# Performance work log

Measured on AMD Instinct MI355X. Metric: run time of the kernel, lower is better.

The kernel has to match this reference:

```python
import jax, jax.numpy as jnp
import numpy as np

ALPHA = 0.2            # LeakyReLU negative slope
N, NFEAT, NHID, NHEADS, NCLASS = 270, 4096, 1024, 8, 8
N_DRUG, N_MIC = 175, 95


def setup_inputs() -> dict:
    key = jax.random.key(0)
    ks = jax.random.split(key, 9)
    return {
        "x": jax.random.normal(ks[0], (N, NFEAT), jnp.float32),
        "adj": jax.random.randint(ks[1], (N, N), 0, 2, jnp.int32),
        # per-head GAT parameters, stacked on a leading head axis
        "W": jax.random.normal(ks[2], (NHEADS, NFEAT, NHID), jnp.float32) * 0.02,
        "a_src": jax.random.normal(ks[3], (NHEADS, NHID), jnp.float32) * 0.02,
        "a_dst": jax.random.normal(ks[4], (NHEADS, NHID), jnp.float32) * 0.02,
        # output attention layer (concat=False)
        "W_out": jax.random.normal(ks[5], (NHEADS * NHID, NCLASS), jnp.float32) * 0.02,
        "a_out_src": jax.random.normal(ks[6], (NCLASS,), jnp.float32) * 0.02,
        "a_out_dst": jax.random.normal(ks[7], (NCLASS,), jnp.float32) * 0.02,
        # bilinear score matrix alpha1 (nclass, nclass)
        "alpha1": jax.random.normal(ks[8], (NCLASS, NCLASS), jnp.float32) * 0.3,
    }


def _gat_layer(h_in, mask, W, a_src, a_dst):
    """pyGAT sparse attention layer, expressed densely with an adjacency mask.

    edge weight e_ij = exp(-leakyrelu(a_src.h_i + a_dst.h_j)) for adj[i,j]!=0,
    h'_i = sum_j e_ij h_j / sum_j e_ij   (dropout=0 -> identity on edge weights)
    """
    h = h_in @ W                                             # (N, D)
    logits = (h @ a_src)[:, None] + (h @ a_dst)[None, :]     # (N, N)
    e = jnp.exp(-jax.nn.leaky_relu(logits, ALPHA)) * mask    # masked edge weights
    return (e @ h) / e.sum(axis=1, keepdims=True)            # (N, D)


def reference(x, adj, W, a_src, a_dst, W_out, a_out_src, a_out_dst, alpha1):
    mask = adj.astype(x.dtype)
    # multi-head attention, concat=True -> elu applied inside each head
    heads = jax.vmap(_gat_layer, in_axes=(None, None, 0, 0, 0))(
        x, mask, W, a_src, a_dst)                            # (H, N, nhid)
    h = jax.nn.elu(heads)
    h = jnp.transpose(h, (1, 0, 2)).reshape(N, NHEADS * NHID)  # torch.cat(dim=1)
    # output attention layer (concat=False), elu applied by SpGAT.forward
    out = jax.nn.elu(_gat_layer(h, mask, W_out, a_out_src, a_out_dst))  # (N, nclass)
    # the 270-iteration python copy loop == a static split at row 175
    drug_k = out[:N_DRUG]                                    # (175, 8)
    mic_k = out[N_DRUG:N_DRUG + N_MIC]                       # (95, 8)
    return (drug_k @ alpha1) @ mic_k.T                       # (175, 95)
```

## Files before the change

kernel.cpp:

```cpp
#include <hip/hip_runtime.h>
#include <hip/hip_bf16.h>

#define NN     270
#define MPAD   320
#define NFEAT  4096
#define NHID   1024
#define NHEADS 8
#define NCLS   8
#define NDRUG  175
#define NMIC   95
#define LALPHA 0.2f

typedef unsigned short u16;
typedef unsigned int   u32;
typedef __attribute__((ext_vector_type(8))) short bf16x8;
typedef __attribute__((ext_vector_type(4))) short bf16x4;
typedef __attribute__((ext_vector_type(4))) float f32x4;

static __device__ __forceinline__ u16 f2bf(float f) {
  union { float f; u32 u; } v; v.f = f;
  u32 r = v.u + 0x7FFFu + ((v.u >> 16) & 1u);
  return (u16)(r >> 16);
}
static __device__ __forceinline__ float bf2f(u16 b) {
  union { u32 u; float f; } v; v.u = ((u32)b) << 16;
  return v.f;
}
static __device__ __forceinline__ float wave_red(float v) {
  #pragma unroll
  for (int o = 32; o > 0; o >>= 1) v += __shfl_down(v, o, 64);
  return v;
}
static __device__ __forceinline__ void block_sync() {
  asm volatile("" ::: "memory");
  __builtin_amdgcn_s_barrier();
  asm volatile("" ::: "memory");
}
#define GLOAD16(g, l) __builtin_amdgcn_global_load_lds(                    \
    (__attribute__((address_space(1))) void*)(g),                          \
    (__attribute__((address_space(3))) void*)(l), 16, 0, 0)

__global__ void cvt_x(const float* __restrict__ x, u16* __restrict__ xb) {
  int i = (blockIdx.x * 256 + threadIdx.x) * 8;
  if (i >= MPAD * NFEAT) return;
  int row = i >> 12;
  uint4 o = {0, 0, 0, 0};
  if (row < NN) {
    float4 a = *(const float4*)(x + i);
    float4 b = *(const float4*)(x + i + 4);
    o.x = (u32)f2bf(a.x) | ((u32)f2bf(a.y) << 16);
    o.y = (u32)f2bf(a.z) | ((u32)f2bf(a.w) << 16);
    o.z = (u32)f2bf(b.x) | ((u32)f2bf(b.y) << 16);
    o.w = (u32)f2bf(b.z) | ((u32)f2bf(b.w) << 16);
  }
  *(uint4*)(xb + i) = o;
}

__global__ __launch_bounds__(256, 2) void gemm1(const u16* __restrict__ xb,
                                                const float* __restrict__ W,
                                                u16* __restrict__ Hpart) {
  __shared__ __align__(16) u16   lA[2][MPAD * 32];
  __shared__ __align__(16) float lWf[3][32 * 64];
  __shared__ __align__(16) u32   lWbf[2][1024];
  const int tid  = threadIdx.x;
  const int lane = tid & 63;
  const int wv   = tid >> 6;
  const int b    = blockIdx.x;
  const int ntile = b >> 2;
  const int ks    = b & 3;
  const int head  = ntile >> 4;
  const int jB    = (ntile & 15) * 64;

  const char* gA0 = (const char*)xb + (tid >> 2) * 8192 + ks * 2048
                    + (((tid & 3) ^ ((tid >> 3) & 3)) << 4);
  const char* gW0 = (const char*)W + (size_t)head * 16777216 + (size_t)ks * 4194304
                    + (tid >> 4) * 4096 + jB * 4 + ((tid & 15) << 4);

  auto issueA = [&](int j) {
    char* l0 = (char*)&lA[j & 1][0] + tid * 16;
    const char* g0 = gA0 + j * 64;
    #pragma unroll
    for (int s = 0; s < 5; ++s)
      GLOAD16(g0 + s * 524288, l0 + s * 4096);
  };
  auto issueW = [&](int j) {
    char* l0 = (char*)&lWf[j % 3][0] + tid * 16;
    const char* g0 = gW0 + j * 131072;
    GLOAD16(g0, l0);
    GLOAD16(g0 + 65536, l0 + 4096);
  };
  const int tcol = tid & 63;
  const int tkb  = tid >> 6;
  auto transposeW = [&](int j) {
    const float* wf = &lWf[j % 3][0];
    float f[8];
    #pragma unroll
    for (int q = 0; q < 8; ++q) f[q] = wf[(tkb * 8 + q) * 64 + tcol];
    uint4 o;
    o.x = (u32)f2bf(f[0]) | ((u32)f2bf(f[1]) << 16);
    o.y = (u32)f2bf(f[2]) | ((u32)f2bf(f[3]) << 16);
    o.z = (u32)f2bf(f[4]) | ((u32)f2bf(f[5]) << 16);
    o.w = (u32)f2bf(f[6]) | ((u32)f2bf(f[7]) << 16);
    *(uint4*)((char*)&lWbf[j & 1][0] + tkb * 1024 + tcol * 16) = o;
  };

  f32x4 acc[5][4];
  #pragma unroll
  for (int m = 0; m < 5; ++m)
    #pragma unroll
    for (int n = 0; n < 4; ++n) acc[m][n] = (f32x4){0.f, 0.f, 0.f, 0.f};

  issueW(0); issueW(1); issueA(0); issueA(1); issueW(2);
  asm volatile("s_waitcnt vmcnt(14)" ::: "memory");
  block_sync();
  transposeW(0);
  asm volatile("s_waitcnt lgkmcnt(0)" ::: "memory");

  const int lc = lane & 15;
  const int lg = lane >> 4;
  for (int j = 0; j < 32; ++j) {
    if (j <= 29)      asm volatile("s_waitcnt vmcnt(7)" ::: "memory");
    else if (j == 30) asm volatile("s_waitcnt vmcnt(5)" ::: "memory");
    else              asm volatile("s_waitcnt vmcnt(0)" ::: "memory");
    block_sync();

    {
      const char* aB = (const char*)&lA[j & 1][0];
      const char* bB = (const char*)&lWbf[j & 1][0];
      bf16x8 bfr[4];
      #pragma unroll
      for (int n = 0; n < 4; ++n)
        bfr[n] = *(const bf16x8*)(bB + lg * 1024 + (n * 16 + lc) * 16);
      #pragma unroll
      for (int m = 0; m < 5; ++m) {
        const int row = wv * 80 + m * 16 + lc;
        bf16x8 afr = *(const bf16x8*)(aB + row * 64 + ((lg ^ ((row >> 1) & 3)) << 4));
        #pragma unroll
        for (int n = 0; n < 4; ++n)
          acc[m][n] = __builtin_amdgcn_mfma_f32_16x16x32_bf16(afr, bfr[n], acc[m][n], 0, 0, 0);
      }
      if (j < 31) transposeW(j + 1);
    }
    asm volatile("s_waitcnt lgkmcnt(0)" ::: "memory");
    block_sync();
    if (j <= 29) issueA(j + 2);
    if (j <= 28) issueW(j + 3);
  }

  u16* hp = Hpart + (size_t)ks * (NN * 8192) + (size_t)(ntile * 64);
  #pragma unroll
  for (int m = 0; m < 5; ++m)
    #pragma unroll
    for (int r = 0; r < 4; ++r) {
      const int row = wv * 80 + m * 16 + (lg << 2) + r;
      if (row < NN) {
        #pragma unroll
        for (int n = 0; n < 4; ++n)
          hp[(size_t)row * 8192 + n * 16 + lc] = f2bf(acc[m][n][r]);
      }
    }
}

__global__ void srcdstf(const u16* __restrict__ Hp, const float* __restrict__ a_src,
                        const float* __restrict__ a_dst, u16* __restrict__ Hb,
                        float* __restrict__ srcv, float* __restrict__ dstv) {
  const int i = blockIdx.x, h = blockIdx.y;
  const int tid = threadIdx.x;
  const int j4 = tid * 4;
  const u16* base = Hp + (size_t)i * 8192 + h * 1024 + j4;
  float4 v = {0.f, 0.f, 0.f, 0.f};
  #pragma unroll
  for (int q = 0; q < 4; ++q) {
    bf16x4 p = *(const bf16x4*)(base + (size_t)q * (NN * 8192));
    v.x += bf2f((u16)p[0]); v.y += bf2f((u16)p[1]);
    v.z += bf2f((u16)p[2]); v.w += bf2f((u16)p[3]);
  }
  u16* hb = Hb + ((size_t)h * NN + i) * NHID + j4;
  ushort4 hv = { f2bf(v.x), f2bf(v.y), f2bf(v.z), f2bf(v.w) };
  *(ushort4*)hb = hv;
  const float4 as4 = *(const float4*)(a_src + h * NHID + j4);
  const float4 ad4 = *(const float4*)(a_dst + h * NHID + j4);
  float s = v.x * as4.x + v.y * as4.y + v.z * as4.z + v.w * as4.w;
  float d = v.x * ad4.x + v.y * ad4.y + v.z * ad4.z + v.w * ad4.w;
  s = wave_red(s); d = wave_red(d);
  __shared__ float rb[8];
  const int lane = tid & 63, wid = tid >> 6;
  if (lane == 0) { rb[wid] = s; rb[4 + wid] = d; }
  __syncthreads();
  if (tid == 0) {
    srcv[h * NN + i] = rb[0] + rb[1] + rb[2] + rb[3];
    dstv[h * NN + i] = rb[4] + rb[5] + rb[6] + rb[7];
  }
}

__global__ void ekern(const int* __restrict__ adj, const float* __restrict__ srcv,
                      const float* __restrict__ dstv, u16* __restrict__ eb,
                      float* __restrict__ rowsum) {
  const int i = blockIdx.x, h = blockIdx.y;
  const int n = threadIdx.x;
  float ev = 0.f;
  if (n < NN && adj[i * NN + n] != 0) {
    float lg = srcv[h * NN + i] + dstv[h * NN + n];
    float lr = lg > 0.f ? lg : LALPHA * lg;
    ev = expf(-lr);
  }
  u16 evb = f2bf(ev);
  eb[(size_t)h * NN * 320 + (size_t)i * 320 + n] = evb;
  float evr = wave_red(bf2f(evb));
  __shared__ float rb[5];
  const int lane = threadIdx.x & 63, wid = threadIdx.x >> 6;
  if (lane == 0) rb[wid] = evr;
  __syncthreads();
  if (threadIdx.x == 0) rowsum[h * NN + i] = rb[0] + rb[1] + rb[2] + rb[3] + rb[4];
}

__global__ __launch_bounds__(512) void gemm2(const u16* __restrict__ eb,
                                             const u16* __restrict__ Hb,
                                             const float* __restrict__ rowsum,
                                             float* __restrict__ h2) {
  __shared__ __align__(16) u16 lA[320 * 72];
  __shared__ __align__(16) u16 lB[32 * 72];
  const int tid  = threadIdx.x;
  const int lane = tid & 63;
  const int wid  = tid >> 6;
  const int wm   = wid >> 1;
  const int wn   = wid & 1;
  const int head = blockIdx.x >> 5;
  const int j0   = (blockIdx.x & 31) * 32;
  f32x4 acc[5];
  #pragma unroll
  for (int m = 0; m < 5; ++m) acc[m] = (f32x4){0.f, 0.f, 0.f, 0.f};

  for (int k0 = 0; k0 < 320; k0 += 64) {
    __syncthreads();
    #pragma unroll
    for (int it = 0; it < 5; ++it) {
      int f   = tid + it * 512;
      int row = f >> 3;
      int kc  = (f & 7) << 3;
      bf16x8 v = {0,0,0,0,0,0,0,0};
      if (row < NN) v = *(const bf16x8*)(eb + (size_t)head * NN * 320 + (size_t)row * 320 + k0 + kc);
      *(bf16x8*)(lA + row * 72 + kc) = v;
    }
    {
      int kk2 = tid >> 3;
      int jc2 = (tid & 7) << 2;
      int k   = k0 + kk2;
      u16 v0 = 0, v1 = 0, v2 = 0, v3 = 0;
      if (k < NN) {
        bf16x4 hv = *(const bf16x4*)(Hb + (size_t)head * NN * NHID + (size_t)k * NHID + j0 + jc2);
        v0 = (u16)hv[0]; v1 = (u16)hv[1]; v2 = (u16)hv[2]; v3 = (u16)hv[3];
      }
      lB[(jc2 + 0) * 72 + kk2] = v0;
      lB[(jc2 + 1) * 72 + kk2] = v1;
      lB[(jc2 + 2) * 72 + kk2] = v2;
      lB[(jc2 + 3) * 72 + kk2] = v3;
    }
    __syncthreads();
    #pragma unroll
    for (int sub = 0; sub < 2; ++sub) {
      int ksub = sub * 32 + ((lane >> 4) << 3);
      bf16x8 bfrag = *(const bf16x8*)(lB + (wn * 16 + (lane & 15)) * 72 + ksub);
      #pragma unroll
      for (int m = 0; m < 5; ++m) {
        int row = wm * 80 + m * 16 + (lane & 15);
        bf16x8 afrag = *(const bf16x8*)(lA + row * 72 + ksub);
        acc[m] = __builtin_amdgcn_mfma_f32_16x16x32_bf16(afrag, bfrag, acc[m], 0, 0, 0);
      }
    }
  }
  const int jj = j0 + wn * 16 + (lane & 15);
  #pragma unroll
  for (int m = 0; m < 5; ++m) {
    #pragma unroll
    for (int r = 0; r < 4; ++r) {
      int row = wm * 80 + m * 16 + ((lane >> 4) << 2) + r;
      if (row < NN) {
        float v = acc[m][r] / rowsum[head * NN + row];
        v = v > 0.f ? v : expm1f(v);
        h2[(size_t)row * (NHEADS * NHID) + head * NHID + jj] = v;
      }
    }
  }
}

__global__ void layer2(const float* __restrict__ h2, const float* __restrict__ Wout,
                       const float* __restrict__ aos, const float* __restrict__ aod,
                       float* __restrict__ hL2, float* __restrict__ src2,
                       float* __restrict__ dst2) {
  const int i = blockIdx.x;
  float acc[8] = {0,0,0,0,0,0,0,0};
  for (int k = threadIdx.x; k < NHEADS * NHID; k += 256) {
    float hv = h2[(size_t)i * (NHEADS * NHID) + k];
    const float4 w0 = *(const float4*)(Wout + (size_t)k * 8);
    const float4 w1 = *(const float4*)(Wout + (size_t)k * 8 + 4);
    acc[0] += hv * w0.x; acc[1] += hv * w0.y; acc[2] += hv * w0.z; acc[3] += hv * w0.w;
    acc[4] += hv * w1.x; acc[5] += hv * w1.y; acc[6] += hv * w1.z; acc[7] += hv * w1.w;
  }
  #pragma unroll
  for (int c = 0; c < 8; ++c) acc[c] = wave_red(acc[c]);
  __shared__ float rb[4][8];
  const int lane = threadIdx.x & 63, wid = threadIdx.x >> 6;
  if (lane == 0) {
    #pragma unroll
    for (int c = 0; c < 8; ++c) rb[wid][c] = acc[c];
  }
  __syncthreads();
  if (threadIdx.x == 0) {
    float s = 0.f, d = 0.f;
    #pragma unroll
    for (int c = 0; c < 8; ++c) {
      float v = rb[0][c] + rb[1][c] + rb[2][c] + rb[3][c];
      hL2[i * 8 + c] = v;
      s += v * aos[c];
      d += v * aod[c];
    }
    src2[i] = s; dst2[i] = d;
  }
}

__global__ void out2k(const int* __restrict__ adj, const float* __restrict__ src2,
                      const float* __restrict__ dst2, const float* __restrict__ hL2,
                      float* __restrict__ out2) {
  const int i = blockIdx.x;
  float se = 0.f, acc[8] = {0,0,0,0,0,0,0,0};
  for (int n = threadIdx.x; n < NN; n += 256) {
    if (adj[i * NN + n] != 0) {
      float lg = src2[i] + dst2[n];
      float lr = lg > 0.f ? lg : LALPHA * lg;
      float ev = expf(-lr);
      se += ev;
      #pragma unroll
      for (int c = 0; c < 8; ++c) acc[c] += ev * hL2[n * 8 + c];
    }
  }
  se = wave_red(se);
  #pragma unroll
  for (int c = 0; c < 8; ++c) acc[c] = wave_red(acc[c]);
  __shared__ float rb[4][9];
  const int lane = threadIdx.x & 63, wid = threadIdx.x >> 6;
  if (lane == 0) {
    #pragma unroll
    for (int c = 0; c < 8; ++c) rb[wid][c] = acc[c];
    rb[wid][8] = se;
  }
  __syncthreads();
  if (threadIdx.x == 0) {
    float s = rb[0][8] + rb[1][8] + rb[2][8] + rb[3][8];
    #pragma unroll
    for (int c = 0; c < 8; ++c) {
      float v = (rb[0][c] + rb[1][c] + rb[2][c] + rb[3][c]) / s;
      out2[i * 8 + c] = v > 0.f ? v : expm1f(v);
    }
  }
}

__global__ void finalk(const float* __restrict__ out2, const float* __restrict__ alpha1,
                       float* __restrict__ out) {
  int t = blockIdx.x * 256 + threadIdx.x;
  if (t >= NDRUG * NMIC) return;
  int d = t / NMIC, m = t % NMIC;
  const float* dr = out2 + d * 8;
  const float* mi = out2 + (NDRUG + m) * 8;
  float r = 0.f;
  #pragma unroll
  for (int c2 = 0; c2 < 8; ++c2) {
    float a = 0.f;
    #pragma unroll
    for (int c1 = 0; c1 < 8; ++c1) a += dr[c1] * alpha1[c1 * 8 + c2];
    r += a * mi[c2];
  }
  out[t] = r;
}

extern "C" void kernel_launch(void* const* d_in, const int* in_sizes, int n_in,
                              void* d_out, int out_size, void* d_ws, size_t ws_size,
                              hipStream_t stream) {
  const float* x      = (const float*)d_in[0];
  const int*   adj    = (const int*)d_in[1];
  const float* W      = (const float*)d_in[2];
  const float* a_src  = (const float*)d_in[3];
  const float* a_dst  = (const float*)d_in[4];
  const float* W_out  = (const float*)d_in[5];
  const float* aos    = (const float*)d_in[6];
  const float* aod    = (const float*)d_in[7];
  const float* alpha1 = (const float*)d_in[8];
  float* out = (float*)d_out;

  char* p = (char*)d_ws;
  auto take = [&](size_t bytes) {
    char* q = p;
    p += (bytes + 255) & ~(size_t)255;
    return q;
  };
  u16*   xb    = (u16*)  take((size_t)MPAD * NFEAT * 2);
  u16*   Hpart = (u16*)  take((size_t)4 * NN * 8192 * 2);
  u16*   Hb    = (u16*)  take((size_t)NHEADS * NN * NHID * 2);
  float* srcv  = (float*)take((size_t)NHEADS * NN * 4);
  float* dstv  = (float*)take((size_t)NHEADS * NN * 4);
  char*  hbase = (char*)Hpart;
  float* h2    = (float*)hbase;
  u16*   eb    = (u16*)  (hbase + 10000000);
  float* rs    = (float*)(hbase + 11500000);
  float* hL2   = (float*)(hbase + 11600000);
  float* s2    = (float*)(hbase + 11700000);
  float* d2    = (float*)(hbase + 11800000);
  float* o2    = (float*)(hbase + 11900000);

  cvt_x<<<640, 256, 0, stream>>>(x, xb);
  gemm1<<<512, 256, 0, stream>>>(xb, W, Hpart);
  srcdstf<<<dim3(NN, NHEADS), 256, 0, stream>>>(Hpart, a_src, a_dst, Hb, srcv, dstv);
  ekern<<<dim3(NN, NHEADS), 320, 0, stream>>>(adj, srcv, dstv, eb, rs);
  gemm2<<<256, 512, 0, stream>>>(eb, Hb, rs, h2);
  layer2<<<NN, 256, 0, stream>>>(h2, W_out, aos, aod, hL2, s2, d2);
  out2k<<<NN, 256, 0, stream>>>(adj, s2, d2, hL2, o2);
  finalk<<<65, 256, 0, stream>>>(o2, alpha1, out);
}
```

Baseline: 91.77 us.

## Split gemm1 M dimension into three 128-row tiles with XCD-aware block mapping

gemm1 now splits the padded 384-row M dimension into three 128-row tiles, with each wave owning a 64x32 sub-tile. This triples the grid to 1536 blocks, lowers per-block LDS and registers, and raises occupancy from 2 to 3 blocks per CU. Blocks are remapped so that all blocks sharing an N tile sit on the same XCD, aiming for better L2 reuse of W. The cost is that W is now fetched three times, once per M tile, and more of the M work is padding (384 rows vs 320).

```diff
diff --git a/kernel.cpp b/kernel.cpp
--- a/kernel.cpp
+++ b/kernel.cpp
@@ -2,7 +2,7 @@
 #include <hip/hip_bf16.h>
 
 #define NN     270
-#define MPAD   320
+#define MPAD   384
 #define NFEAT  4096
 #define NHID   1024
 #define NHEADS 8
@@ -56,32 +56,37 @@
   *(uint4*)(xb + i) = o;
 }
 
-__global__ __launch_bounds__(256, 2) void gemm1(const u16* __restrict__ xb,
+__global__ __launch_bounds__(256, 3) void gemm1(const u16* __restrict__ xb,
                                                 const float* __restrict__ W,
                                                 u16* __restrict__ Hpart) {
-  __shared__ __align__(16) u16   lA[2][MPAD * 32];
+  __shared__ __align__(16) u16   lA[2][128 * 32];
   __shared__ __align__(16) float lWf[3][32 * 64];
   __shared__ __align__(16) u32   lWbf[2][1024];
   const int tid  = threadIdx.x;
   const int lane = tid & 63;
   const int wv   = tid >> 6;
-  const int b    = blockIdx.x;
-  const int ntile = b >> 2;
-  const int ks    = b & 3;
+  const int wm   = wv >> 1;
+  const int wn   = wv & 1;
+  const int bid   = blockIdx.x;
+  const int xcd   = bid & 7;
+  const int local = bid >> 3;
+  const int ntile = xcd * 16 + local / 12;
+  const int r12   = local % 12;
+  const int mt    = r12 % 3;
+  const int ks    = r12 / 3;
   const int head  = ntile >> 4;
   const int jB    = (ntile & 15) * 64;
 
-  const char* gA0 = (const char*)xb + (tid >> 2) * 8192 + ks * 2048
-                    + (((tid & 3) ^ ((tid >> 3) & 3)) << 4);
+  const char* gA0 = (const char*)xb + (size_t)(mt * 128 + (tid >> 2)) * 8192
+                    + ks * 2048 + (((tid & 3) ^ ((tid >> 3) & 3)) << 4);
   const char* gW0 = (const char*)W + (size_t)head * 16777216 + (size_t)ks * 4194304
                     + (tid >> 4) * 4096 + jB * 4 + ((tid & 15) << 4);
 
   auto issueA = [&](int j) {
     char* l0 = (char*)&lA[j & 1][0] + tid * 16;
     const char* g0 = gA0 + j * 64;
-    #pragma unroll
-    for (int s = 0; s < 5; ++s)
-      GLOAD16(g0 + s * 524288, l0 + s * 4096);
+    GLOAD16(g0, l0);
+    GLOAD16(g0 + 524288, l0 + 4096);
   };
   auto issueW = [&](int j) {
     char* l0 = (char*)&lWf[j % 3][0] + tid * 16;
@@ -104,14 +109,14 @@
     *(uint4*)((char*)&lWbf[j & 1][0] + tkb * 1024 + tcol * 16) = o;
   };
 
-  f32x4 acc[5][4];
-  #pragma unroll
-  for (int m = 0; m < 5; ++m)
-    #pragma unroll
-    for (int n = 0; n < 4; ++n) acc[m][n] = (f32x4){0.f, 0.f, 0.f, 0.f};
+  f32x4 acc[4][2];
+  #pragma unroll
+  for (int m = 0; m < 4; ++m)
+    #pragma unroll
+    for (int n = 0; n < 2; ++n) acc[m][n] = (f32x4){0.f, 0.f, 0.f, 0.f};
 
   issueW(0); issueW(1); issueA(0); issueA(1); issueW(2);
-  asm volatile("s_waitcnt vmcnt(14)" ::: "memory");
+  asm volatile("s_waitcnt vmcnt(8)" ::: "memory");
   block_sync();
   transposeW(0);
   asm volatile("s_waitcnt lgkmcnt(0)" ::: "memory");
@@ -119,24 +124,24 @@
   const int lc = lane & 15;
   const int lg = lane >> 4;
   for (int j = 0; j < 32; ++j) {
-    if (j <= 29)      asm volatile("s_waitcnt vmcnt(7)" ::: "memory");
-    else if (j == 30) asm volatile("s_waitcnt vmcnt(5)" ::: "memory");
+    if (j <= 29)      asm volatile("s_waitcnt vmcnt(4)" ::: "memory");
+    else if (j == 30) asm volatile("s_waitcnt vmcnt(2)" ::: "memory");
     else              asm volatile("s_waitcnt vmcnt(0)" ::: "memory");
     block_sync();
 
     {
       const char* aB = (const char*)&lA[j & 1][0];
       const char* bB = (const char*)&lWbf[j & 1][0];
-      bf16x8 bfr[4];
+      bf16x8 bfr[2];
       #pragma unroll
-      for (int n = 0; n < 4; ++n)
-        bfr[n] = *(const bf16x8*)(bB + lg * 1024 + (n * 16 + lc) * 16);
+      for (int n = 0; n < 2; ++n)
+        bfr[n] = *(const bf16x8*)(bB + lg * 1024 + (wn * 32 + n * 16 + lc) * 16);
       #pragma unroll
-      for (int m = 0; m < 5; ++m) {
-        const int row = wv * 80 + m * 16 + lc;
+      for (int m = 0; m < 4; ++m) {
+        const int row = wm * 64 + m * 16 + lc;
         bf16x8 afr = *(const bf16x8*)(aB + row * 64 + ((lg ^ ((row >> 1) & 3)) << 4));
         #pragma unroll
-        for (int n = 0; n < 4; ++n)
+        for (int n = 0; n < 2; ++n)
           acc[m][n] = __builtin_amdgcn_mfma_f32_16x16x32_bf16(afr, bfr[n], acc[m][n], 0, 0, 0);
       }
       if (j < 31) transposeW(j + 1);
@@ -147,15 +152,15 @@
     if (j <= 28) issueW(j + 3);
   }
 
-  u16* hp = Hpart + (size_t)ks * (NN * 8192) + (size_t)(ntile * 64);
-  #pragma unroll
-  for (int m = 0; m < 5; ++m)
+  u16* hp = Hpart + (size_t)ks * (NN * 8192) + (size_t)(ntile * 64) + wn * 32;
+  #pragma unroll
+  for (int m = 0; m < 4; ++m)
     #pragma unroll
     for (int r = 0; r < 4; ++r) {
-      const int row = wv * 80 + m * 16 + (lg << 2) + r;
+      const int row = mt * 128 + wm * 64 + m * 16 + (lg << 2) + r;
       if (row < NN) {
         #pragma unroll
-        for (int n = 0; n < 4; ++n)
+        for (int n = 0; n < 2; ++n)
           hp[(size_t)row * 8192 + n * 16 + lc] = f2bf(acc[m][n][r]);
       }
     }
@@ -407,8 +412,8 @@
   float* d2    = (float*)(hbase + 11800000);
   float* o2    = (float*)(hbase + 11900000);
 
-  cvt_x<<<640, 256, 0, stream>>>(x, xb);
-  gemm1<<<512, 256, 0, stream>>>(xb, W, Hpart);
+  cvt_x<<<768, 256, 0, stream>>>(x, xb);
+  gemm1<<<1536, 256, 0, stream>>>(xb, W, Hpart);
   srcdstf<<<dim3(NN, NHEADS), 256, 0, stream>>>(Hpart, a_src, a_dst, Hb, srcv, dstv);
   ekern<<<dim3(NN, NHEADS), 320, 0, stream>>>(adj, srcv, dstv, eb, rs);
   gemm2<<<256, 512, 0, stream>>>(eb, Hb, rs, h2);
```

Measured after the change: 110.3 us. 20.2% more time.

## Retile gemm1 to 256-wide N tiles with 8-way K split and register-staged W

Applied to the files above, without the earlier changes.

Restructures the main x@W GEMM. Blocks now have 512 threads and cover a 320x256 output tile, with the K dimension split 8 ways instead of 4 and the grid halved. W is no longer staged through LDS as fp32 and transposed there. Each thread loads 16 fp32 W values into registers, double-buffered across iterations, then converts them to bf16 and writes them to LDS. The intent is to reuse each A tile across more output columns and drop the fp32 LDS staging, at the cost of more partial sums for srcdstf to reduce, more registers per thread, and a full vmcnt(0) wait every iteration.

```diff
diff --git a/kernel.cpp b/kernel.cpp
--- a/kernel.cpp
+++ b/kernel.cpp
@@ -10,6 +10,7 @@
 #define NDRUG  175
 #define NMIC   95
 #define LALPHA 0.2f
+#define NKS    8
 
 typedef unsigned short u16;
 typedef unsigned int   u32;
@@ -34,6 +35,9 @@
 static __device__ __forceinline__ void block_sync() {
   asm volatile("" ::: "memory");
   __builtin_amdgcn_s_barrier();
+  asm volatile("" ::: "memory");
+}
+static __device__ __forceinline__ void compiler_fence() {
   asm volatile("" ::: "memory");
 }
 #define GLOAD16(g, l) __builtin_amdgcn_global_load_lds(                    \
@@ -56,106 +60,125 @@
   *(uint4*)(xb + i) = o;
 }
 
-__global__ __launch_bounds__(256, 2) void gemm1(const u16* __restrict__ xb,
-                                                const float* __restrict__ W,
-                                                u16* __restrict__ Hpart) {
-  __shared__ __align__(16) u16   lA[2][MPAD * 32];
-  __shared__ __align__(16) float lWf[3][32 * 64];
-  __shared__ __align__(16) u32   lWbf[2][1024];
+__global__ __launch_bounds__(512) void gemm1(const u16* __restrict__ xb,
+                                             const float* __restrict__ W,
+                                             u16* __restrict__ Hpart) {
+  __shared__ __align__(16) u16 lA[2][MPAD * 32];
+  __shared__ __align__(16) u32 lWbf[2][4096];
   const int tid  = threadIdx.x;
   const int lane = tid & 63;
   const int wv   = tid >> 6;
-  const int b    = blockIdx.x;
-  const int ntile = b >> 2;
-  const int ks    = b & 3;
-  const int head  = ntile >> 4;
-  const int jB    = (ntile & 15) * 64;
-
-  const char* gA0 = (const char*)xb + (tid >> 2) * 8192 + ks * 2048
-                    + (((tid & 3) ^ ((tid >> 3) & 3)) << 4);
-  const char* gW0 = (const char*)W + (size_t)head * 16777216 + (size_t)ks * 4194304
-                    + (tid >> 4) * 4096 + jB * 4 + ((tid & 15) << 4);
+  const int wm   = wv >> 1;
+  const int wn   = wv & 1;
+  const int lc   = lane & 15;
+  const int lg   = lane >> 4;
+  const int ks    = blockIdx.x & 7;
+  const int ntile = blockIdx.x >> 3;
+  const int head  = ntile >> 2;
+  const int jB    = (ntile & 3) * 256;
 
   auto issueA = [&](int j) {
-    char* l0 = (char*)&lA[j & 1][0] + tid * 16;
-    const char* g0 = gA0 + j * 64;
-    #pragma unroll
-    for (int s = 0; s < 5; ++s)
-      GLOAD16(g0 + s * 524288, l0 + s * 4096);
+    char* lbase = (char*)&lA[j & 1][0];
+    #pragma unroll
+    for (int q = 0; q < 2; ++q) {
+      int c = q * 512 + tid;
+      int row = c >> 2, p = c & 3;
+      const char* g = (const char*)xb + (size_t)row * 8192 + ks * 1024 + j * 64
+                      + ((p ^ ((row >> 1) & 3)) << 4);
+      GLOAD16(g, lbase + c * 16);
+    }
+    if (tid < 256) {
+      int c = 1024 + tid;
+      int row = c >> 2, p = c & 3;
+      const char* g = (const char*)xb + (size_t)row * 8192 + ks * 1024 + j * 64
+                      + ((p ^ ((row >> 1) & 3)) << 4);
+      GLOAD16(g, lbase + c * 16);
+    }
   };
-  auto issueW = [&](int j) {
-    char* l0 = (char*)&lWf[j % 3][0] + tid * 16;
-    const char* g0 = gW0 + j * 131072;
-    GLOAD16(g0, l0);
-    GLOAD16(g0 + 65536, l0 + 4096);
-  };
-  const int tcol = tid & 63;
-  const int tkb  = tid >> 6;
-  auto transposeW = [&](int j) {
-    const float* wf = &lWf[j % 3][0];
-    float f[8];
-    #pragma unroll
-    for (int q = 0; q < 8; ++q) f[q] = wf[(tkb * 8 + q) * 64 + tcol];
-    uint4 o;
-    o.x = (u32)f2bf(f[0]) | ((u32)f2bf(f[1]) << 16);
-    o.y = (u32)f2bf(f[2]) | ((u32)f2bf(f[3]) << 16);
-    o.z = (u32)f2bf(f[4]) | ((u32)f2bf(f[5]) << 16);
-    o.w = (u32)f2bf(f[6]) | ((u32)f2bf(f[7]) << 16);
-    *(uint4*)((char*)&lWbf[j & 1][0] + tkb * 1024 + tcol * 16) = o;
-  };
-
-  f32x4 acc[5][4];
+
+  const float* wbase = W + (size_t)head * 4194304
+                       + ((size_t)ks * 512 + (size_t)(tid >> 8) * 16) * 1024
+                       + jB + (tid & 255);
+  #define LOADW(J, WR)                                                     \
+    { const float* ws_ = wbase + (size_t)(J) * 32768;                      \
+      _Pragma("unroll")                                                    \
+      for (int q_ = 0; q_ < 16; ++q_) WR[q_] = ws_[(size_t)q_ * 1024]; }
+
+  const int wcol = tid & 255;
+  const int wkh  = tid >> 8;
+  #define CVTW(DSTBUF, WR)                                                 \
+    { u32* d_ = &lWbf[DSTBUF][0];                                          \
+      _Pragma("unroll")                                                    \
+      for (int i_ = 0; i_ < 2; ++i_) {                                     \
+        int kb_ = wkh * 2 + i_;                                            \
+        uint4 o_;                                                          \
+        o_.x = (u32)f2bf(WR[i_*8+0]) | ((u32)f2bf(WR[i_*8+1]) << 16);      \
+        o_.y = (u32)f2bf(WR[i_*8+2]) | ((u32)f2bf(WR[i_*8+3]) << 16);      \
+        o_.z = (u32)f2bf(WR[i_*8+4]) | ((u32)f2bf(WR[i_*8+5]) << 16);      \
+        o_.w = (u32)f2bf(WR[i_*8+6]) | ((u32)f2bf(WR[i_*8+7]) << 16);      \
+        *(uint4*)((char*)d_ + (kb_ * 256 + wcol) * 16) = o_;               \
+      } }
+
+  f32x4 acc[5][8];
   #pragma unroll
   for (int m = 0; m < 5; ++m)
     #pragma unroll
-    for (int n = 0; n < 4; ++n) acc[m][n] = (f32x4){0.f, 0.f, 0.f, 0.f};
-
-  issueW(0); issueW(1); issueA(0); issueA(1); issueW(2);
-  asm volatile("s_waitcnt vmcnt(14)" ::: "memory");
-  block_sync();
-  transposeW(0);
+    for (int n = 0; n < 8; ++n) acc[m][n] = (f32x4){0.f, 0.f, 0.f, 0.f};
+
+  float wA[16], wB[16];
+  issueA(0); issueA(1);
+  compiler_fence();
+  LOADW(0, wA); LOADW(1, wB);
+  asm volatile("s_waitcnt vmcnt(16)" ::: "memory");
+  CVTW(0, wA);
   asm volatile("s_waitcnt lgkmcnt(0)" ::: "memory");
 
-  const int lc = lane & 15;
-  const int lg = lane >> 4;
-  for (int j = 0; j < 32; ++j) {
-    if (j <= 29)      asm volatile("s_waitcnt vmcnt(7)" ::: "memory");
-    else if (j == 30) asm volatile("s_waitcnt vmcnt(5)" ::: "memory");
-    else              asm volatile("s_waitcnt vmcnt(0)" ::: "memory");
-    block_sync();
-
-    {
-      const char* aB = (const char*)&lA[j & 1][0];
-      const char* bB = (const char*)&lWbf[j & 1][0];
-      bf16x8 bfr[4];
-      #pragma unroll
-      for (int n = 0; n < 4; ++n)
-        bfr[n] = *(const bf16x8*)(bB + lg * 1024 + (n * 16 + lc) * 16);
-      #pragma unroll
-      for (int m = 0; m < 5; ++m) {
-        const int row = wv * 80 + m * 16 + lc;
-        bf16x8 afr = *(const bf16x8*)(aB + row * 64 + ((lg ^ ((row >> 1) & 3)) << 4));
-        #pragma unroll
-        for (int n = 0; n < 4; ++n)
-          acc[m][n] = __builtin_amdgcn_mfma_f32_16x16x32_bf16(afr, bfr[n], acc[m][n], 0, 0, 0);
-      }
-      if (j < 31) transposeW(j + 1);
-    }
-    asm volatile("s_waitcnt lgkmcnt(0)" ::: "memory");
-    block_sync();
-    if (j <= 29) issueA(j + 2);
-    if (j <= 28) issueW(j + 3);
-  }
-
-  u16* hp = Hpart + (size_t)ks * (NN * 8192) + (size_t)(ntile * 64);
+  #define BODY(J, WCVT, WLOAD)                                             \
+    {                                                                      \
+      const int j_ = (J);                                                  \
+      block_sync();            \
+      const char* aB = (const char*)&lA[j_ & 1][0];                        \
+      const char* bB = (const char*)&lWbf[j_ & 1][0];                      \
+      bf16x8 bfr[8];                                                       \
+      _Pragma("unroll")                                                    \
+      for (int n = 0; n < 8; ++n) {                                        \
+        int col = wn * 128 + n * 16 + lc;                                  \
+        bfr[n] = *(const bf16x8*)(bB + ((lg * 256 + col) << 4));           \
+      }                                                                    \
+      _Pragma("unroll")                                                    \
+      for (int m = 0; m < 5; ++m) {                                        \
+        int row = wm * 80 + m * 16 + lc;                                   \
+        bf16x8 afr = *(const bf16x8*)(aB + row * 64                        \
+                       + ((lg ^ ((row >> 1) & 3)) << 4));                  \
+        _Pragma("unroll")                                                  \
+        for (int n = 0; n < 8; ++n)                                        \
+          acc[m][n] = __builtin_amdgcn_mfma_f32_16x16x32_bf16(             \
+              afr, bfr[n], acc[m][n], 0, 0, 0);                            \
+      }                                                                    \
+      asm volatile("s_waitcnt vmcnt(0)" ::: "memory");                     \
+      if (j_ < 15) { CVTW((j_ + 1) & 1, WCVT); }                           \
+      asm volatile("s_waitcnt lgkmcnt(0)" ::: "memory");                   \
+      block_sync();        \
+      if (j_ < 14) { issueA(j_ + 2); LOADW(j_ + 2, WLOAD); }               \
+    }
+
+  for (int jj = 0; jj < 16; jj += 2) {
+    BODY(jj,     wB, wA);
+    BODY(jj + 1, wA, wB);
+  }
+  #undef BODY
+  #undef LOADW
+  #undef CVTW
+
+  u16* hp = Hpart + (size_t)ks * (NN * 8192) + ntile * 256 + wn * 128;
   #pragma unroll
   for (int m = 0; m < 5; ++m)
     #pragma unroll
     for (int r = 0; r < 4; ++r) {
-      const int row = wv * 80 + m * 16 + (lg << 2) + r;
+      const int row = wm * 80 + m * 16 + (lg << 2) + r;
       if (row < NN) {
         #pragma unroll
-        for (int n = 0; n < 4; ++n)
+        for (int n = 0; n < 8; ++n)
           hp[(size_t)row * 8192 + n * 16 + lc] = f2bf(acc[m][n][r]);
       }
     }
@@ -170,7 +193,7 @@
   const u16* base = Hp + (size_t)i * 8192 + h * 1024 + j4;
   float4 v = {0.f, 0.f, 0.f, 0.f};
   #pragma unroll
-  for (int q = 0; q < 4; ++q) {
+  for (int q = 0; q < NKS; ++q) {
     bf16x4 p = *(const bf16x4*)(base + (size_t)q * (NN * 8192));
     v.x += bf2f((u16)p[0]); v.y += bf2f((u16)p[1]);
     v.z += bf2f((u16)p[2]); v.w += bf2f((u16)p[3]);
@@ -394,7 +417,7 @@
     return q;
   };
   u16*   xb    = (u16*)  take((size_t)MPAD * NFEAT * 2);
-  u16*   Hpart = (u16*)  take((size_t)4 * NN * 8192 * 2);
+  u16*   Hpart = (u16*)  take((size_t)NKS * NN * 8192 * 2);
   u16*   Hb    = (u16*)  take((size_t)NHEADS * NN * NHID * 2);
   float* srcv  = (float*)take((size_t)NHEADS * NN * 4);
   float* dstv  = (float*)take((size_t)NHEADS * NN * 4);
@@ -408,7 +431,7 @@
   float* o2    = (float*)(hbase + 11900000);
 
   cvt_x<<<640, 256, 0, stream>>>(x, xb);
-  gemm1<<<512, 256, 0, stream>>>(xb, W, Hpart);
+  gemm1<<<256, 512, 0, stream>>>(xb, W, Hpart);
   srcdstf<<<dim3(NN, NHEADS), 256, 0, stream>>>(Hpart, a_src, a_dst, Hb, srcv, dstv);
   ekern<<<dim3(NN, NHEADS), 320, 0, stream>>>(adj, srcv, dstv, eb, rs);
   gemm2<<<256, 512, 0, stream>>>(eb, Hb, rs, h2);
```

New measurement: 95.55 us. +4.1%, slower.

## Widen gemm1 tiles to 256 columns with 8-way split-K and 512-thread blocks

Applied to the files above, without the earlier changes.

Restructures the first GEMM so each 512-thread block computes a 320x256 output tile, with 8 waves in a 4x2 layout, instead of 320x64 with 4 waves. The K dimension is split 8 ways instead of 4. Each staged A tile of x is now reused across four times as many output columns, which cuts redundant A loads and per-column-tile overhead. The cost is more split-K partial buffers that srcdstf must sum, more LDS per block, more accumulator registers per thread, and a shorter pipeline with W double-buffered instead of triple-buffered.

```diff
diff --git a/kernel.cpp b/kernel.cpp
--- a/kernel.cpp
+++ b/kernel.cpp
@@ -10,6 +10,7 @@
 #define NDRUG  175
 #define NMIC   95
 #define LALPHA 0.2f
+#define NKS    8
 
 typedef unsigned short u16;
 typedef unsigned int   u32;
@@ -56,106 +57,136 @@
   *(uint4*)(xb + i) = o;
 }
 
-__global__ __launch_bounds__(256, 2) void gemm1(const u16* __restrict__ xb,
-                                                const float* __restrict__ W,
-                                                u16* __restrict__ Hpart) {
+__global__ __launch_bounds__(512) void gemm1(const u16* __restrict__ xb,
+                                             const float* __restrict__ W,
+                                             u16* __restrict__ Hpart) {
   __shared__ __align__(16) u16   lA[2][MPAD * 32];
-  __shared__ __align__(16) float lWf[3][32 * 64];
-  __shared__ __align__(16) u32   lWbf[2][1024];
+  __shared__ __align__(16) float lWf[2][32 * 256];
+  __shared__ __align__(16) u32   lWbf[2][4096];
   const int tid  = threadIdx.x;
   const int lane = tid & 63;
   const int wv   = tid >> 6;
-  const int b    = blockIdx.x;
-  const int ntile = b >> 2;
-  const int ks    = b & 3;
-  const int head  = ntile >> 4;
-  const int jB    = (ntile & 15) * 64;
-
-  const char* gA0 = (const char*)xb + (tid >> 2) * 8192 + ks * 2048
-                    + (((tid & 3) ^ ((tid >> 3) & 3)) << 4);
-  const char* gW0 = (const char*)W + (size_t)head * 16777216 + (size_t)ks * 4194304
-                    + (tid >> 4) * 4096 + jB * 4 + ((tid & 15) << 4);
+  const int wm   = wv >> 1;
+  const int wn   = wv & 1;
+  const int lc   = lane & 15;
+  const int lg   = lane >> 4;
+  const int ks    = blockIdx.x & 7;
+  const int ntile = blockIdx.x >> 3;
+  const int head  = ntile >> 2;
+  const int jB    = (ntile & 3) * 256;
 
   auto issueA = [&](int j) {
-    char* l0 = (char*)&lA[j & 1][0] + tid * 16;
-    const char* g0 = gA0 + j * 64;
-    #pragma unroll
-    for (int s = 0; s < 5; ++s)
-      GLOAD16(g0 + s * 524288, l0 + s * 4096);
+    char* lbase = (char*)&lA[j & 1][0];
+    #pragma unroll
+    for (int q = 0; q < 2; ++q) {
+      int c = q * 512 + tid;
+      int row = c >> 2, p = c & 3;
+      const char* g = (const char*)xb + (size_t)row * 8192 + ks * 1024 + j * 64
+                      + ((p ^ ((row >> 1) & 3)) << 4);
+      GLOAD16(g, lbase + c * 16);
+    }
+    if (tid < 256) {
+      int c = 1024 + tid;
+      int row = c >> 2, p = c & 3;
+      const char* g = (const char*)xb + (size_t)row * 8192 + ks * 1024 + j * 64
+                      + ((p ^ ((row >> 1) & 3)) << 4);
+      GLOAD16(g, lbase + c * 16);
+    }
   };
+
+  const char* gW0 = (const char*)(W + (size_t)head * 4194304
+                                    + (size_t)ks * 512 * 1024 + jB);
   auto issueW = [&](int j) {
-    char* l0 = (char*)&lWf[j % 3][0] + tid * 16;
-    const char* g0 = gW0 + j * 131072;
-    GLOAD16(g0, l0);
-    GLOAD16(g0 + 65536, l0 + 4096);
+    char* l0 = (char*)&lWf[j & 1][0] + tid * 16;
+    const char* g0 = gW0 + (size_t)j * 131072 + (tid >> 6) * 4096 + (lane << 4);
+    #pragma unroll
+    for (int q = 0; q < 4; ++q)
+      GLOAD16(g0 + q * 32768, l0 + q * 8192);
   };
-  const int tcol = tid & 63;
-  const int tkb  = tid >> 6;
-  auto transposeW = [&](int j) {
-    const float* wf = &lWf[j % 3][0];
-    float f[8];
-    #pragma unroll
-    for (int q = 0; q < 8; ++q) f[q] = wf[(tkb * 8 + q) * 64 + tcol];
-    uint4 o;
-    o.x = (u32)f2bf(f[0]) | ((u32)f2bf(f[1]) << 16);
-    o.y = (u32)f2bf(f[2]) | ((u32)f2bf(f[3]) << 16);
-    o.z = (u32)f2bf(f[4]) | ((u32)f2bf(f[5]) << 16);
-    o.w = (u32)f2bf(f[6]) | ((u32)f2bf(f[7]) << 16);
-    *(uint4*)((char*)&lWbf[j & 1][0] + tkb * 1024 + tcol * 16) = o;
+
+  const int wcol = tid & 255;
+  const int wkb0 = (tid >> 8) * 2;
+  auto transposeW = [&](int t) {
+    const float* wf = &lWf[t & 1][0];
+    u32* dst = &lWbf[t & 1][0];
+    #pragma unroll
+    for (int i2 = 0; i2 < 2; ++i2) {
+      int kb = wkb0 + i2;
+      float f[8];
+      #pragma unroll
+      for (int q = 0; q < 8; ++q) f[q] = wf[(kb * 8 + q) * 256 + wcol];
+      uint4 o;
+      o.x = (u32)f2bf(f[0]) | ((u32)f2bf(f[1]) << 16);
+      o.y = (u32)f2bf(f[2]) | ((u32)f2bf(f[3]) << 16);
+      o.z = (u32)f2bf(f[4]) | ((u32)f2bf(f[5]) << 16);
+      o.w = (u32)f2bf(f[6]) | ((u32)f2bf(f[7]) << 16);
+      *(uint4*)((char*)dst + (kb * 256 + wcol) * 16) = o;
+    }
   };
 
-  f32x4 acc[5][4];
+  #define WAITV(N03, N47)                                                  \
+    do {                                                                   \
+      if (wv < 4) asm volatile("s_waitcnt vmcnt(" #N03 ")" ::: "memory");  \
+      else        asm volatile("s_waitcnt vmcnt(" #N47 ")" ::: "memory");  \
+    } while (0)
+
+  f32x4 acc[5][8];
   #pragma unroll
   for (int m = 0; m < 5; ++m)
     #pragma unroll
-    for (int n = 0; n < 4; ++n) acc[m][n] = (f32x4){0.f, 0.f, 0.f, 0.f};
-
-  issueW(0); issueW(1); issueA(0); issueA(1); issueW(2);
-  asm volatile("s_waitcnt vmcnt(14)" ::: "memory");
+    for (int n = 0; n < 8; ++n) acc[m][n] = (f32x4){0.f, 0.f, 0.f, 0.f};
+
+  issueW(0); issueW(1); issueA(0); issueA(1);
+  WAITV(10, 8);
   block_sync();
   transposeW(0);
   asm volatile("s_waitcnt lgkmcnt(0)" ::: "memory");
-
-  const int lc = lane & 15;
-  const int lg = lane >> 4;
-  for (int j = 0; j < 32; ++j) {
-    if (j <= 29)      asm volatile("s_waitcnt vmcnt(7)" ::: "memory");
-    else if (j == 30) asm volatile("s_waitcnt vmcnt(5)" ::: "memory");
-    else              asm volatile("s_waitcnt vmcnt(0)" ::: "memory");
+  block_sync();
+  issueW(2);
+
+  for (int j = 0; j < 16; ++j) {
+    if (j <= 13) {
+      WAITV(7, 6);
+    } else if (j == 14) {
+      WAITV(3, 2);
+    } else {
+      asm volatile("s_waitcnt vmcnt(0)" ::: "memory");
+    }
     block_sync();
 
-    {
-      const char* aB = (const char*)&lA[j & 1][0];
-      const char* bB = (const char*)&lWbf[j & 1][0];
-      bf16x8 bfr[4];
+    const char* aB = (const char*)&lA[j & 1][0];
+    const char* bB = (const char*)&lWbf[j & 1][0];
+    bf16x8 bfr[8];
+    #pragma unroll
+    for (int n = 0; n < 8; ++n) {
+      int col = wn * 128 + n * 16 + lc;
+      bfr[n] = *(const bf16x8*)(bB + ((lg * 256 + col) << 4));
+    }
+    #pragma unroll
+    for (int m = 0; m < 5; ++m) {
+      int row = wm * 80 + m * 16 + lc;
+      bf16x8 afr = *(const bf16x8*)(aB + row * 64 + ((lg ^ ((row >> 1) & 3)) << 4));
       #pragma unroll
-      for (int n = 0; n < 4; ++n)
-        bfr[n] = *(const bf16x8*)(bB + lg * 1024 + (n * 16 + lc) * 16);
-      #pragma unroll
-      for (int m = 0; m < 5; ++m) {
-        const int row = wv * 80 + m * 16 + lc;
-        bf16x8 afr = *(const bf16x8*)(aB + row * 64 + ((lg ^ ((row >> 1) & 3)) << 4));
-        #pragma unroll
-        for (int n = 0; n < 4; ++n)
-          acc[m][n] = __builtin_amdgcn_mfma_f32_16x16x32_bf16(afr, bfr[n], acc[m][n], 0, 0, 0);
-      }
-      if (j < 31) transposeW(j + 1);
-    }
+      for (int n = 0; n < 8; ++n)
+        acc[m][n] = __builtin_amdgcn_mfma_f32_16x16x32_bf16(afr, bfr[n], acc[m][n], 0, 0, 0);
+    }
+    if (j < 15) transposeW(j + 1);
     asm volatile("s_waitcnt lgkmcnt(0)" ::: "memory");
     block_sync();
-    if (j <= 29) issueA(j + 2);
-    if (j <= 28) issueW(j + 3);
-  }
-
-  u16* hp = Hpart + (size_t)ks * (NN * 8192) + (size_t)(ntile * 64);
+    if (j <= 13) issueA(j + 2);
+    if (j <= 12) issueW(j + 3);
+  }
+  #undef WAITV
+
+  u16* hp = Hpart + (size_t)ks * (NN * 8192) + ntile * 256 + wn * 128;
   #pragma unroll
   for (int m = 0; m < 5; ++m)
     #pragma unroll
     for (int r = 0; r < 4; ++r) {
-      const int row = wv * 80 + m * 16 + (lg << 2) + r;
+      const int row = wm * 80 + m * 16 + (lg << 2) + r;
       if (row < NN) {
         #pragma unroll
-        for (int n = 0; n < 4; ++n)
+        for (int n = 0; n < 8; ++n)
           hp[(size_t)row * 8192 + n * 16 + lc] = f2bf(acc[m][n][r]);
       }
     }
@@ -170,7 +201,7 @@
   const u16* base = Hp + (size_t)i * 8192 + h * 1024 + j4;
   float4 v = {0.f, 0.f, 0.f, 0.f};
   #pragma unroll
-  for (int q = 0; q < 4; ++q) {
+  for (int q = 0; q < NKS; ++q) {
     bf16x4 p = *(const bf16x4*)(base + (size_t)q * (NN * 8192));
     v.x += bf2f((u16)p[0]); v.y += bf2f((u16)p[1]);
     v.z += bf2f((u16)p[2]); v.w += bf2f((u16)p[3]);
@@ -394,7 +425,7 @@
     return q;
   };
   u16*   xb    = (u16*)  take((size_t)MPAD * NFEAT * 2);
-  u16*   Hpart = (u16*)  take((size_t)4 * NN * 8192 * 2);
+  u16*   Hpart = (u16*)  take((size_t)NKS * NN * 8192 * 2);
   u16*   Hb    = (u16*)  take((size_t)NHEADS * NN * NHID * 2);
   float* srcv  = (float*)take((size_t)NHEADS * NN * 4);
   float* dstv  = (float*)take((size_t)NHEADS * NN * 4);
@@ -408,7 +439,7 @@
   float* o2    = (float*)(hbase + 11900000);
 
   cvt_x<<<640, 256, 0, stream>>>(x, xb);
-  gemm1<<<512, 256, 0, stream>>>(xb, W, Hpart);
+  gemm1<<<256, 512, 0, stream>>>(xb, W, Hpart);
   srcdstf<<<dim3(NN, NHEADS), 256, 0, stream>>>(Hpart, a_src, a_dst, Hb, srcv, dstv);
   ekern<<<dim3(NN, NHEADS), 320, 0, stream>>>(adj, srcv, dstv, eb, rs);
   gemm2<<<256, 512, 0, stream>>>(eb, Hb, rs, h2);
```

New measurement: 92.40 us. Within noise of the previous version (+0.7%).
